# Kernel tuning notes

Measured on AMD Instinct MI355X. Metric: run time of the kernel, lower is better.

Reference implementation:

```python
import jax, jax.numpy as jnp
import numpy as np
import math

GRID_H, GRID_W = 128, 128
INIT_LENGTHSCALE = 0.1

def make_grid(h, w):
    yy, xx = jnp.meshgrid(jnp.arange(h, dtype=jnp.float32) / h,
                          jnp.arange(w, dtype=jnp.float32) / w, indexing='ij')
    return jnp.stack([xx, yy], axis=-1)  # [H, W, 2]

def setup_inputs() -> dict:
    key = jax.random.key(0)
    k1, k2 = jax.random.split(key)
    B, N, C = 8, 2048, 3
    return {
        'x_context': jax.random.uniform(k1, (B, N, 2), dtype=jnp.float32),
        'y_context': jax.random.normal(k2, (B, N, C), dtype=jnp.float32),
        'context_mask': jnp.ones((B, N), dtype=jnp.float32),
        'log_lengthscale': jnp.asarray(math.log(INIT_LENGTHSCALE), dtype=jnp.float32),
        'grid': make_grid(GRID_H, GRID_W),
    }

def reference(x_context, y_context, context_mask, log_lengthscale, grid):
    B = x_context.shape[0]
    H, W = grid.shape[0], grid.shape[1]
    grid_flat = grid.reshape(-1, 2)  # [HW, 2]
    # squared pairwise distances: [B, HW, N]
    sq_dist = jnp.sum((grid_flat[None, :, None, :] - x_context[:, None, :, :]) ** 2, axis=-1)
    lengthscale = jnp.exp(log_lengthscale)
    weights = jnp.exp(-0.5 * sq_dist / (lengthscale ** 2))
    weights = weights * context_mask[:, None, :]
    signal = jnp.einsum('bgn,bnc->bgc', weights, y_context)  # [B, HW, C]
    density = jnp.sum(weights, axis=-1, keepdims=True)        # [B, HW, 1]
    grid_repr = jnp.concatenate([signal, density], axis=-1).reshape(B, H, W, -1)
    return jnp.transpose(grid_repr, (0, 3, 1, 2))  # [B, C+1, H, W]
```

## Files before the change

### kernel.cpp

```cpp
#include <hip/hip_runtime.h>
#include <math.h>


constexpr int BB = 8;
constexpr int NN = 2048;
constexpr int GH = 128;
constexpr int GW = 128;
constexpr int GY_TILE = 16;
constexpr int KSPLIT  = 8;
constexpr int NK = NN / KSPLIT;
constexpr int NC = 32;
constexpr int OUTSZ = BB * 4 * GH * GW;

__device__ __forceinline__ int swz_col(int gx) {
    int g = gx >> 2;
    return (((g ^ ((g >> 4) & 1)) << 2) | (gx & 3));
}

template <bool ATOMIC>
__global__ __launch_bounds__(256, 2) void setconv_fused(
    const float* __restrict__ xc,
    const float* __restrict__ yc,
    const float* __restrict__ mask,
    const float* __restrict__ logls,
    const float* __restrict__ grid,
    float* __restrict__ dst)
{
    __shared__ float sEX[NC][GW];
    __shared__ float sYT[NC][GY_TILE][4];

    const int ks  = blockIdx.x;
    const int gyt = blockIdx.y;
    const int b   = blockIdx.z;
    const int tid = threadIdx.x;
    const int tx  = tid & 15;
    const int ty  = tid >> 4;

    const float ls = __expf(logls[0]);
    const float cc = -0.72134752044f / (ls * ls);

    const int n_base = ks * NK;

    const int   gxs  = tid & 127;
    const int   hi   = tid >> 7;
    const float gxv  = grid[gxs * 2 + 0];
    const int   colx = swz_col(gxs);
    const int   gyl  = tid & 15;
    const int   nlo  = tid >> 4;
    const float gyv  = grid[((gyt * GY_TILE + gyl) * GW) * 2 + 1];

    const int colA = swz_col(tx * 8);
    const int colB = swz_col(tx * 8 + 4);

    float acc[8][4];
#pragma unroll
    for (int j = 0; j < 8; ++j)
#pragma unroll
        for (int c = 0; c < 4; ++c) acc[j][c] = 0.0f;

    for (int ch = 0; ch < NK; ch += NC) {
        __syncthreads();

#pragma unroll
        for (int r = 0; r < (NC * GW) / 256; ++r) {
            int nl = 2 * r + hi;
            int n  = n_base + ch + nl;
            float xn = xc[(b * NN + n) * 2 + 0];
            float dx = gxv - xn;
            sEX[nl][colx] = exp2f(cc * dx * dx);
        }
#pragma unroll
        for (int r = 0; r < (NC * GY_TILE) / 256; ++r) {
            int nl = r * 16 + nlo;
            int n  = n_base + ch + nl;
            float yn  = xc[(b * NN + n) * 2 + 1];
            float dy  = gyv - yn;
            float ey  = exp2f(cc * dy * dy);
            float m   = mask[b * NN + n];
            float eym = ey * m;
            sYT[nl][gyl][0] = eym * yc[(b * NN + n) * 3 + 0];
            sYT[nl][gyl][1] = eym * yc[(b * NN + n) * 3 + 1];
            sYT[nl][gyl][2] = eym * yc[(b * NN + n) * 3 + 2];
            sYT[nl][gyl][3] = eym;
        }
        __syncthreads();

#pragma unroll
        for (int nl = 0; nl < NC; ++nl) {
            float4 yt = *(const float4*)&sYT[nl][ty][0];
            float4 ea = *(const float4*)&sEX[nl][colA];
            float4 eb = *(const float4*)&sEX[nl][colB];
            float ex[8] = {ea.x, ea.y, ea.z, ea.w, eb.x, eb.y, eb.z, eb.w};
#pragma unroll
            for (int j = 0; j < 8; ++j) {
                acc[j][0] = fmaf(ex[j], yt.x, acc[j][0]);
                acc[j][1] = fmaf(ex[j], yt.y, acc[j][1]);
                acc[j][2] = fmaf(ex[j], yt.z, acc[j][2]);
                acc[j][3] = fmaf(ex[j], yt.w, acc[j][3]);
            }
        }
    }

    const int gy = gyt * GY_TILE + ty;
    if (ATOMIC) {
#pragma unroll
        for (int c = 0; c < 4; ++c)
#pragma unroll
            for (int j = 0; j < 8; ++j)
                atomicAdd(&dst[(((b * 4 + c) * GH) + gy) * GW + tx * 8 + j],
                          acc[j][c]);
    } else {
        float* slice = dst + (size_t)ks * OUTSZ;
#pragma unroll
        for (int c = 0; c < 4; ++c) {
            int base = (((b * 4 + c) * GH) + gy) * GW + tx * 8;
            float4 v0 = {acc[0][c], acc[1][c], acc[2][c], acc[3][c]};
            float4 v1 = {acc[4][c], acc[5][c], acc[6][c], acc[7][c]};
            *(float4*)&slice[base]     = v0;
            *(float4*)&slice[base + 4] = v1;
        }
    }
}

__global__ __launch_bounds__(256) void setconv_reduce(
    const float* __restrict__ pw,
    float* __restrict__ out)
{
    const int n4 = OUTSZ / 4;
    int i = blockIdx.x * 256 + threadIdx.x;
    if (i >= n4) return;
    const float4* p = (const float4*)pw;
    float4 s = p[i];
#pragma unroll
    for (int k = 1; k < KSPLIT; ++k) {
        float4 v = p[(size_t)k * n4 + i];
        s.x += v.x; s.y += v.y; s.z += v.z; s.w += v.w;
    }
    ((float4*)out)[i] = s;
}

extern "C" void kernel_launch(void* const* d_in, const int* in_sizes, int n_in,
                              void* d_out, int out_size, void* d_ws, size_t ws_size,
                              hipStream_t stream) {
    const float* xc    = (const float*)d_in[0];
    const float* yc    = (const float*)d_in[1];
    const float* mask  = (const float*)d_in[2];
    const float* logls = (const float*)d_in[3];
    const float* grid  = (const float*)d_in[4];
    float* out = (float*)d_out;

    dim3 grid_dim(KSPLIT, GH / GY_TILE, BB);
    const size_t need = (size_t)KSPLIT * OUTSZ * sizeof(float);

    if (ws_size >= need) {
        float* pw = (float*)d_ws;
        setconv_fused<false><<<grid_dim, 256, 0, stream>>>(xc, yc, mask, logls,
                                                           grid, pw);
        setconv_reduce<<<dim3(OUTSZ / 4 / 256), 256, 0, stream>>>(pw, out);
    } else {
        hipMemsetAsync(out, 0, (size_t)out_size * sizeof(float), stream);
        setconv_fused<true><<<grid_dim, 256, 0, stream>>>(xc, yc, mask, logls,
                                                          grid, out);
    }
}
```

Measured before the change: 102.9 us.

## Compute separable Gaussian contraction with split-bf16 MFMA instead of FP32 FMAs

Replaces the FP32 outer-product FMA loop with bf16 MFMA 16x16x32 instructions. Each FP32 operand is split into high and low bf16 parts, and three MFMAs per tile are used to recover near-FP32 accuracy. The x-exp and y-exp·value factors are computed per lane straight into the fragment layout in shared memory with vectorized loads. The reduce kernel becomes grid-stride with 512 blocks. This adds conversion overhead and output stores that are less coalesced, and it risks small accuracy loss from the bf16 split.

```diff
diff --git a/kernel.cpp b/kernel.cpp
--- a/kernel.cpp
+++ b/kernel.cpp
@@ -1,24 +1,34 @@
 #include <hip/hip_runtime.h>
+#include <hip/hip_bf16.h>
 #include <math.h>
 
 
-constexpr int BB = 8;
-constexpr int NN = 2048;
-constexpr int GH = 128;
-constexpr int GW = 128;
+typedef float f32x4 __attribute__((ext_vector_type(4)));
+typedef short s16x8 __attribute__((ext_vector_type(8)));
+
+constexpr int BB = 8, NN = 2048, GH = 128, GW = 128;
 constexpr int GY_TILE = 16;
 constexpr int KSPLIT  = 8;
-constexpr int NK = NN / KSPLIT;
-constexpr int NC = 32;
-constexpr int OUTSZ = BB * 4 * GH * GW;
-
-__device__ __forceinline__ int swz_col(int gx) {
-    int g = gx >> 2;
-    return (((g ^ ((g >> 4) & 1)) << 2) | (gx & 3));
+constexpr int NK      = NN / KSPLIT;
+constexpr int NCH     = NK / 32;
+constexpr int OUTSZ   = BB * 4 * GH * GW;
+
+__device__ __forceinline__ void split2(float v0, float v1,
+                                       unsigned& hi, unsigned& lo) {
+    __hip_bfloat16 a = __float2bfloat16(v0);
+    __hip_bfloat16 b = __float2bfloat16(v1);
+    float fa = __bfloat162float(a), fb = __bfloat162float(b);
+    __hip_bfloat16 ra = __float2bfloat16(v0 - fa);
+    __hip_bfloat16 rb = __float2bfloat16(v1 - fb);
+    unsigned short ua, ub, uc, ud;
+    __builtin_memcpy(&ua, &a, 2);  __builtin_memcpy(&ub, &b, 2);
+    __builtin_memcpy(&uc, &ra, 2); __builtin_memcpy(&ud, &rb, 2);
+    hi = (unsigned)ua | ((unsigned)ub << 16);
+    lo = (unsigned)uc | ((unsigned)ud << 16);
 }
 
 template <bool ATOMIC>
-__global__ __launch_bounds__(256, 2) void setconv_fused(
+__global__ __launch_bounds__(256, 2) void setconv_mfma(
     const float* __restrict__ xc,
     const float* __restrict__ yc,
     const float* __restrict__ mask,
@@ -26,117 +36,143 @@
     const float* __restrict__ grid,
     float* __restrict__ dst)
 {
-    __shared__ float sEX[NC][GW];
-    __shared__ float sYT[NC][GY_TILE][4];
+    __shared__ unsigned sA[2][4 * 64 * 4];
+    __shared__ unsigned sB[2][8 * 64 * 4];
 
     const int ks  = blockIdx.x;
     const int gyt = blockIdx.y;
     const int b   = blockIdx.z;
     const int tid = threadIdx.x;
-    const int tx  = tid & 15;
-    const int ty  = tid >> 4;
+    const int l   = tid & 63;
+    const int w   = tid >> 6;
 
     const float ls = __expf(logls[0]);
     const float cc = -0.72134752044f / (ls * ls);
 
-    const int n_base = ks * NK;
-
-    const int   gxs  = tid & 127;
-    const int   hi   = tid >> 7;
-    const float gxv  = grid[gxs * 2 + 0];
-    const int   colx = swz_col(gxs);
-    const int   gyl  = tid & 15;
-    const int   nlo  = tid >> 4;
-    const float gyv  = grid[((gyt * GY_TILE + gyl) * GW) * 2 + 1];
-
-    const int colA = swz_col(tx * 8);
-    const int colB = swz_col(tx * 8 + 4);
-
-    float acc[8][4];
-#pragma unroll
-    for (int j = 0; j < 8; ++j)
-#pragma unroll
-        for (int c = 0; c < 4; ++c) acc[j][c] = 0.0f;
-
-    for (int ch = 0; ch < NK; ch += NC) {
+    const int lane_s = tid >> 2;
+    const int jp     = tid & 3;
+    const int sb15   = lane_s & 15;
+    const int kg     = lane_s >> 4;
+    const int k0     = ((jp >> 1) << 4) | (kg << 2) | ((jp & 1) << 1);
+    const int ch     = sb15 & 3;
+    const int gyb    = sb15 >> 2;
+
+    float gxv[8];
+#pragma unroll
+    for (int r = 0; r < 8; ++r) gxv[r] = grid[(r * 16 + sb15) * 2 + 0];
+    float gyv[4];
+#pragma unroll
+    for (int r = 0; r < 4; ++r)
+        gyv[r] = grid[(size_t)(gyt * GY_TILE + r * 4 + gyb) * GW * 2 + 1];
+
+    const int mtb = (w & 1) * 2;
+    const int ntb = (w >> 1) * 4;
+
+    f32x4 acc[2][4];
+#pragma unroll
+    for (int i = 0; i < 2; ++i)
+#pragma unroll
+        for (int j = 0; j < 4; ++j) acc[i][j] = (f32x4){0.f, 0.f, 0.f, 0.f};
+
+    const int nb0 = b * NN + ks * NK;
+
+    for (int chn = 0; chn < NCH; ++chn) {
+        const int kbase = nb0 + chn * 32 + k0;
+        const float4 xy = *(const float4*)&xc[(size_t)kbase * 2];
+        const float2 mk = *(const float2*)&mask[kbase];
+        float yv0 = 0.f, yv1 = 0.f;
+        if (ch < 3) {
+            yv0 = yc[(size_t)kbase * 3 + ch];
+            yv1 = yc[(size_t)(kbase + 1) * 3 + ch];
+        }
+        const float y40 = (ch < 3) ? yv0 * mk.x : mk.x;
+        const float y41 = (ch < 3) ? yv1 * mk.y : mk.y;
+
         __syncthreads();
 
 #pragma unroll
-        for (int r = 0; r < (NC * GW) / 256; ++r) {
-            int nl = 2 * r + hi;
-            int n  = n_base + ch + nl;
-            float xn = xc[(b * NN + n) * 2 + 0];
-            float dx = gxv - xn;
-            sEX[nl][colx] = exp2f(cc * dx * dx);
-        }
-#pragma unroll
-        for (int r = 0; r < (NC * GY_TILE) / 256; ++r) {
-            int nl = r * 16 + nlo;
-            int n  = n_base + ch + nl;
-            float yn  = xc[(b * NN + n) * 2 + 1];
-            float dy  = gyv - yn;
-            float ey  = exp2f(cc * dy * dy);
-            float m   = mask[b * NN + n];
-            float eym = ey * m;
-            sYT[nl][gyl][0] = eym * yc[(b * NN + n) * 3 + 0];
-            sYT[nl][gyl][1] = eym * yc[(b * NN + n) * 3 + 1];
-            sYT[nl][gyl][2] = eym * yc[(b * NN + n) * 3 + 2];
-            sYT[nl][gyl][3] = eym;
+        for (int r = 0; r < 8; ++r) {
+            float d0 = gxv[r] - xy.x, d1 = gxv[r] - xy.z;
+            float v0 = exp2f(cc * d0 * d0), v1 = exp2f(cc * d1 * d1);
+            unsigned hi, lo;
+            split2(v0, v1, hi, lo);
+            sB[0][r * 256 + tid] = hi;
+            sB[1][r * 256 + tid] = lo;
+        }
+#pragma unroll
+        for (int r = 0; r < 4; ++r) {
+            float d0 = gyv[r] - xy.y, d1 = gyv[r] - xy.w;
+            float e0 = exp2f(cc * d0 * d0) * y40;
+            float e1 = exp2f(cc * d1 * d1) * y41;
+            unsigned hi, lo;
+            split2(e0, e1, hi, lo);
+            sA[0][r * 256 + tid] = hi;
+            sA[1][r * 256 + tid] = lo;
         }
         __syncthreads();
 
-#pragma unroll
-        for (int nl = 0; nl < NC; ++nl) {
-            float4 yt = *(const float4*)&sYT[nl][ty][0];
-            float4 ea = *(const float4*)&sEX[nl][colA];
-            float4 eb = *(const float4*)&sEX[nl][colB];
-            float ex[8] = {ea.x, ea.y, ea.z, ea.w, eb.x, eb.y, eb.z, eb.w};
-#pragma unroll
-            for (int j = 0; j < 8; ++j) {
-                acc[j][0] = fmaf(ex[j], yt.x, acc[j][0]);
-                acc[j][1] = fmaf(ex[j], yt.y, acc[j][1]);
-                acc[j][2] = fmaf(ex[j], yt.z, acc[j][2]);
-                acc[j][3] = fmaf(ex[j], yt.w, acc[j][3]);
+        const s16x8* pAh = (const s16x8*)sA[0];
+        const s16x8* pAl = (const s16x8*)sA[1];
+        const s16x8* pBh = (const s16x8*)sB[0];
+        const s16x8* pBl = (const s16x8*)sB[1];
+        s16x8 ah[2], al[2], bh[4], bl[4];
+#pragma unroll
+        for (int i = 0; i < 2; ++i) {
+            ah[i] = pAh[(mtb + i) * 64 + l];
+            al[i] = pAl[(mtb + i) * 64 + l];
+        }
+#pragma unroll
+        for (int j = 0; j < 4; ++j) {
+            bh[j] = pBh[(ntb + j) * 64 + l];
+            bl[j] = pBl[(ntb + j) * 64 + l];
+        }
+#pragma unroll
+        for (int i = 0; i < 2; ++i)
+#pragma unroll
+            for (int j = 0; j < 4; ++j) {
+                acc[i][j] = __builtin_amdgcn_mfma_f32_16x16x32_bf16(
+                    ah[i], bh[j], acc[i][j], 0, 0, 0);
+                acc[i][j] = __builtin_amdgcn_mfma_f32_16x16x32_bf16(
+                    ah[i], bl[j], acc[i][j], 0, 0, 0);
+                acc[i][j] = __builtin_amdgcn_mfma_f32_16x16x32_bf16(
+                    al[i], bh[j], acc[i][j], 0, 0, 0);
             }
-        }
-    }
-
-    const int gy = gyt * GY_TILE + ty;
-    if (ATOMIC) {
-#pragma unroll
-        for (int c = 0; c < 4; ++c)
-#pragma unroll
-            for (int j = 0; j < 8; ++j)
-                atomicAdd(&dst[(((b * 4 + c) * GH) + gy) * GW + tx * 8 + j],
-                          acc[j][c]);
-    } else {
-        float* slice = dst + (size_t)ks * OUTSZ;
-#pragma unroll
-        for (int c = 0; c < 4; ++c) {
-            int base = (((b * 4 + c) * GH) + gy) * GW + tx * 8;
-            float4 v0 = {acc[0][c], acc[1][c], acc[2][c], acc[3][c]};
-            float4 v1 = {acc[4][c], acc[5][c], acc[6][c], acc[7][c]};
-            *(float4*)&slice[base]     = v0;
-            *(float4*)&slice[base + 4] = v1;
-        }
-    }
-}
-
-__global__ __launch_bounds__(256) void setconv_reduce(
+    }
+
+    const int colg = l & 15, rowg = l >> 4;
+    float* slice = ATOMIC ? dst : dst + (size_t)ks * OUTSZ;
+#pragma unroll
+    for (int i = 0; i < 2; ++i) {
+        const int gy = gyt * GY_TILE + (mtb + i) * 4 + rowg;
+#pragma unroll
+        for (int j = 0; j < 4; ++j) {
+            const int gx = (ntb + j) * 16 + colg;
+#pragma unroll
+            for (int r = 0; r < 4; ++r) {
+                const size_t off = (((size_t)(b * 4 + r)) * GH + gy) * GW + gx;
+                if (ATOMIC) atomicAdd(&slice[off], acc[i][j][r]);
+                else        slice[off] = acc[i][j][r];
+            }
+        }
+    }
+}
+
+__global__ __launch_bounds__(256, 8) void setconv_reduce(
     const float* __restrict__ pw,
     float* __restrict__ out)
 {
     const int n4 = OUTSZ / 4;
-    int i = blockIdx.x * 256 + threadIdx.x;
-    if (i >= n4) return;
+    const int stride = gridDim.x * 256;
     const float4* p = (const float4*)pw;
-    float4 s = p[i];
-#pragma unroll
-    for (int k = 1; k < KSPLIT; ++k) {
-        float4 v = p[(size_t)k * n4 + i];
-        s.x += v.x; s.y += v.y; s.z += v.z; s.w += v.w;
-    }
-    ((float4*)out)[i] = s;
+    for (int i = blockIdx.x * 256 + threadIdx.x; i < n4; i += stride) {
+        float4 s = p[i];
+#pragma unroll
+        for (int k = 1; k < KSPLIT; ++k) {
+            float4 v = p[(size_t)k * n4 + i];
+            s.x += v.x; s.y += v.y; s.z += v.z; s.w += v.w;
+        }
+        ((float4*)out)[i] = s;
+    }
 }
 
 extern "C" void kernel_launch(void* const* d_in, const int* in_sizes, int n_in,
@@ -149,17 +185,17 @@
     const float* grid  = (const float*)d_in[4];
     float* out = (float*)d_out;
 
-    dim3 grid_dim(KSPLIT, GH / GY_TILE, BB);
+    dim3 gdim(KSPLIT, GH / GY_TILE, BB);
     const size_t need = (size_t)KSPLIT * OUTSZ * sizeof(float);
 
     if (ws_size >= need) {
         float* pw = (float*)d_ws;
-        setconv_fused<false><<<grid_dim, 256, 0, stream>>>(xc, yc, mask, logls,
-                                                           grid, pw);
-        setconv_reduce<<<dim3(OUTSZ / 4 / 256), 256, 0, stream>>>(pw, out);
+        setconv_mfma<false><<<gdim, 256, 0, stream>>>(xc, yc, mask, logls,
+                                                      grid, pw);
+        setconv_reduce<<<dim3(512), 256, 0, stream>>>(pw, out);
     } else {
         hipMemsetAsync(out, 0, (size_t)out_size * sizeof(float), stream);
-        setconv_fused<true><<<grid_dim, 256, 0, stream>>>(xc, yc, mask, logls,
-                                                          grid, out);
-    }
-}
+        setconv_mfma<true><<<gdim, 256, 0, stream>>>(xc, yc, mask, logls,
+                                                     grid, out);
+    }
+}
```

New measurement: 89.43 us. -13.1%, faster.
